# Kernel tuning notes

Hardware: AMD Instinct MI355X
Metric: run time of the kernel (lower is better)

Reference implementation:

```python
import jax, jax.numpy as jnp
import numpy as np

D = 768  # BERT hidden / GCN feature dim


def gcn_conv(x, src, dst, W, b, num_nodes):
    """PyG GCNConv: add self-loops, symmetric normalization, x @ W, scatter-sum, + bias."""
    loop = jnp.arange(num_nodes, dtype=src.dtype)
    s = jnp.concatenate([src, loop])
    d = jnp.concatenate([dst, loop])
    deg = jax.ops.segment_sum(jnp.ones_like(d, dtype=x.dtype), d, num_segments=num_nodes)
    dis = jax.lax.rsqrt(deg)  # deg >= 1 due to self-loops
    norm = dis[s] * dis[d]  # [E+N]
    h = x @ W  # [N, out]
    msg = h[s] * norm[:, None]  # [E+N, out] -- largest intermediate
    return jax.ops.segment_sum(msg, d, num_segments=num_nodes) + b


def setup_inputs() -> dict:
    key = jax.random.key(0)
    ks = jax.random.split(key, 12)
    B, N, E, K = 64, 50000, 500000, 20
    inp = {
        "query_bert_embedding": jax.random.normal(ks[0], (B, D), jnp.float32),
        "names_bert_embedding": jax.random.normal(ks[1], (N, D), jnp.float32),
        "sparse_score": jax.random.uniform(ks[2], (B, N), jnp.float32),
        "query_indices": jax.random.randint(ks[3], (B,), 0, N, jnp.int32),
        "edge_index": jax.random.randint(ks[4], (2, E), 0, N, jnp.int32),
        "sparse_weight": jnp.ones((1,), jnp.float32),
        "W1": jax.random.normal(ks[5], (D, D), jnp.float32) * (1.0 / np.sqrt(D)),
        "b1": jnp.zeros((D,), jnp.float32),
        "W2": jax.random.normal(ks[6], (D, D), jnp.float32) * (1.0 / np.sqrt(D)),
        "b2": jnp.zeros((D,), jnp.float32),
        "score_W": jax.random.normal(ks[7], (2 * D, 1), jnp.float32) * (1.0 / np.sqrt(2 * D)),
        "score_b": jnp.zeros((1,), jnp.float32),
        "top_k": K,
    }
    return inp


def reference(query_bert_embedding, names_bert_embedding, sparse_score, query_indices,
              edge_index, sparse_weight, W1, b1, W2, b2, score_W, score_b, top_k):
    N = names_bert_embedding.shape[0]
    src, dst = edge_index[0], edge_index[1]

    # two-layer GraphSAGE (GCNConv) over the name graph (dropout omitted for determinism)
    g = gcn_conv(names_bert_embedding, src, dst, W1, b1, N)
    g = jax.nn.relu(g)
    names_graph_embedding = gcn_conv(g, src, dst, W2, b2, N)  # [N, D]

    # candidate retrieval (torch.no_grad in original)
    bert_score = query_bert_embedding @ names_bert_embedding.T  # [B, N]
    score_full = jax.lax.stop_gradient(sparse_weight[0] * sparse_score + bert_score)
    _, candidates_indices = jax.lax.top_k(score_full, top_k)  # [B, K]

    # training: force gold index into candidate list (replace last slot if absent)
    qi = query_indices.astype(candidates_indices.dtype)
    contains = jnp.any(candidates_indices == qi[:, None], axis=1)  # [B]
    candidates_indices = candidates_indices.at[:, -1].set(
        jnp.where(contains, candidates_indices[:, -1], qi))

    # vectorized per-candidate gather + concat + Linear(1536->1) + ReLU
    cand_g = names_graph_embedding[candidates_indices]  # [B, K, D]
    B, K = candidates_indices.shape
    q = jnp.broadcast_to(query_bert_embedding[:, None, :], (B, K, D))
    feat = jnp.concatenate([cand_g, q], axis=-1)  # [B, K, 2D]
    score = jax.nn.relu(jnp.squeeze(feat @ score_W, -1) + score_b[0])  # [B, K]
    return score, candidates_indices
```

## Files before the change

kernel.cpp:

```cpp
#include <hip/hip_runtime.h>
#include <stdint.h>

#define D 768
#define FCH 16
#define CPC 16
#define NCAND 256

typedef __bf16 bf16x8 __attribute__((ext_vector_type(8)));
typedef float  f32x4  __attribute__((ext_vector_type(4)));
typedef float  f32x2  __attribute__((ext_vector_type(2)));

static __device__ __forceinline__ float b2f(unsigned short u){
    union { unsigned int i; float f; } v; v.i = ((unsigned int)u) << 16; return v.f;
}
static __device__ __forceinline__ unsigned short f2b(float f){
    union { float f; unsigned int i; } v; v.f = f;
    unsigned int u = v.i;
    unsigned int r = (u + 0x7fffu + ((u >> 16) & 1u)) >> 16;
    return (unsigned short)r;
}
static __device__ __forceinline__ void gload_lds16(const void* g, void* l){
    __builtin_amdgcn_global_load_lds((const __attribute__((address_space(1))) void*)g,
                                     (__attribute__((address_space(3))) void*)l, 16, 0, 0);
}
static __device__ __forceinline__ void dec4_fma(unsigned int u, float nm, float* acc){
    f32x2 a = __builtin_amdgcn_cvt_pk_f32_fp8((int)u, false);
    f32x2 b = __builtin_amdgcn_cvt_pk_f32_fp8((int)u, true);
    acc[0] += a[0] * nm; acc[1] += a[1] * nm;
    acc[2] += b[0] * nm; acc[3] += b[1] * nm;
}
static __device__ __forceinline__ unsigned char f2fp8(float f){
    int p = __builtin_amdgcn_cvt_pk_fp8_f32(f, 0.0f, 0, false);
    return (unsigned char)(p & 0xFF);
}
static __device__ __forceinline__ unsigned int pk4_fp8(float a, float b, float c, float d){
    int lo = __builtin_amdgcn_cvt_pk_fp8_f32(a, b, 0, false);
    int fu = __builtin_amdgcn_cvt_pk_fp8_f32(c, d, lo, true);
    return (unsigned int)fu;
}

__global__ __launch_bounds__(256) void cvt8_kernel(const float* __restrict__ x,
                                                   unsigned char* __restrict__ y8, size_t n){
    size_t i = ((size_t)blockIdx.x * 256 + threadIdx.x) * 4;
    if (i + 3 < n){
        f32x4 v = *(const f32x4*)(x + i);
        *(unsigned int*)(y8 + i) = pk4_fp8(v[0], v[1], v[2], v[3]);
    }
}

__global__ __launch_bounds__(256) void transposeW8(const float* __restrict__ W,
                                                   unsigned char* __restrict__ Wt){
    __shared__ unsigned char tile[32][33];
    int bx = blockIdx.x * 32;
    int by = blockIdx.y * 32;
    int tx = threadIdx.x & 31, ty = threadIdx.x >> 5;
    #pragma unroll
    for (int r = 0; r < 32; r += 8)
        tile[ty + r][tx] = f2fp8(W[(size_t)(bx + ty + r) * D + by + tx]);
    __syncthreads();
    #pragma unroll
    for (int r = 0; r < 32; r += 8)
        Wt[(size_t)(by + ty + r) * D + bx + tx] = tile[tx][ty + r];
}

__global__ __launch_bounds__(256) void deg_count(const int* __restrict__ dst, int* cnt, int E){
    int e = blockIdx.x * 256 + threadIdx.x;
    if (e < E) atomicAdd(&cnt[dst[e]], 1);
}
__global__ __launch_bounds__(256) void dis_blocksum(const int* __restrict__ cnt,
                                                    float* __restrict__ dis,
                                                    int* __restrict__ bsum, int N){
    __shared__ int sm[256];
    int tid = threadIdx.x;
    int i = blockIdx.x * 256 + tid;
    int c = (i < N) ? cnt[i] : 0;
    if (i < N) dis[i] = rsqrtf((float)(c + 1));
    sm[tid] = c;
    __syncthreads();
    for (int o = 128; o > 0; o >>= 1){
        if (tid < o) sm[tid] += sm[tid + o];
        __syncthreads();
    }
    if (tid == 0) bsum[blockIdx.x] = sm[0];
}
__global__ __launch_bounds__(256) void scanb_k(const int* __restrict__ bsum, int* boff, int nb){
    __shared__ int sm[256];
    int tid = threadIdx.x;
    int v = (tid < nb) ? bsum[tid] : 0;
    sm[tid] = v;
    __syncthreads();
    for (int o = 1; o < 256; o <<= 1){
        int add = (tid >= o) ? sm[tid - o] : 0;
        __syncthreads();
        sm[tid] += add;
        __syncthreads();
    }
    if (tid < nb) boff[tid] = sm[tid] - v;
}
__global__ __launch_bounds__(256) void scanfin_k(const int* __restrict__ cnt,
                                                 const int* __restrict__ boff,
                                                 int* start, int* fill, int N, int E){
    __shared__ int sm[256];
    int tid = threadIdx.x;
    int i = blockIdx.x * 256 + tid;
    int v = (i < N) ? cnt[i] : 0;
    sm[tid] = v;
    __syncthreads();
    for (int o = 1; o < 256; o <<= 1){
        int add = (tid >= o) ? sm[tid - o] : 0;
        __syncthreads();
        sm[tid] += add;
        __syncthreads();
    }
    if (i < N){ start[i] = boff[blockIdx.x] + sm[tid] - v; fill[i] = 0; }
    if (i == 0) start[N] = E;
}
__global__ __launch_bounds__(256) void csr_fill(const int* __restrict__ src,
                                                const int* __restrict__ dst,
                                                const float* __restrict__ dis,
                                                const int* __restrict__ start,
                                                int* fill, int* csr_src, float* csr_norm, int E){
    int e = blockIdx.x * 256 + threadIdx.x;
    if (e >= E) return;
    int s = src[e], d = dst[e];
    int pos = atomicAdd(&fill[d], 1);
    int idx = start[d] + pos;
    csr_src[idx]  = s;
    csr_norm[idx] = dis[s] * dis[d];
}

__global__ __launch_bounds__(256) void gemm_fp8(const unsigned char* __restrict__ A,
                                                const unsigned char* __restrict__ Bt,
                                                unsigned char* __restrict__ Cout,
                                                int M, int nTilesN){
    __shared__ unsigned char Al[128 * 32];
    __shared__ unsigned char Bl[128 * 32];
    const int nwg = gridDim.x;
    const int bid = blockIdx.x;
    const int q = nwg >> 3, r = nwg & 7;
    const int xcd = bid & 7, loc = bid >> 3;
    const int swz = (xcd < r ? xcd * (q + 1) : r * (q + 1) + (xcd - r) * q) + loc;
    const int mt = swz / nTilesN, nt = swz % nTilesN;
    const int m0 = mt * 128, n0 = nt * 128;

    const int tid  = threadIdx.x;
    const int lane = tid & 63;
    const int w    = tid >> 6;
    const int wr = w >> 1, wc = w & 1;
    const int l15 = lane & 15;
    const int lg  = lane >> 4;

    const int g     = w * 64 + lane;
    const int srow  = g >> 1;
    const int shalf = (g & 1) * 16;

    f32x4 acc[4][4] = {};

    for (int k0 = 0; k0 < D; k0 += 32){
        gload_lds16(A  + (size_t)(m0 + srow) * D + k0 + shalf, (char*)Al + w * 1024);
        gload_lds16(Bt + (size_t)(n0 + srow) * D + k0 + shalf, (char*)Bl + w * 1024);
        __syncthreads();
        long af[4], bfv[4];
        #pragma unroll
        for (int mf = 0; mf < 4; mf++)
            af[mf] = *(const long*)(&Al[(wr * 64 + mf * 16 + l15) * 32 + lg * 8]);
        #pragma unroll
        for (int nf = 0; nf < 4; nf++)
            bfv[nf] = *(const long*)(&Bl[(wc * 64 + nf * 16 + l15) * 32 + lg * 8]);
        #pragma unroll
        for (int mf = 0; mf < 4; mf++)
            #pragma unroll
            for (int nf = 0; nf < 4; nf++)
                acc[mf][nf] = __builtin_amdgcn_mfma_f32_16x16x32_fp8_fp8(af[mf], bfv[nf], acc[mf][nf], 0, 0, 0);
        __syncthreads();
    }
    #pragma unroll
    for (int mf = 0; mf < 4; mf++){
        #pragma unroll
        for (int r2 = 0; r2 < 4; r2++){
            int gr = m0 + wr * 64 + mf * 16 + lg * 4 + r2;
            if (gr < M){
                #pragma unroll
                for (int nf = 0; nf < 4; nf++){
                    int gc = n0 + wc * 64 + nf * 16 + l15;
                    Cout[(size_t)gr * D + gc] = f2fp8(acc[mf][nf][r2]);
                }
            }
        }
    }
}

__global__ __launch_bounds__(256) void gemm_fp8_list(const unsigned char* __restrict__ A,
                                                     const unsigned char* __restrict__ Bt,
                                                     unsigned char* __restrict__ Cout,
                                                     const int* __restrict__ RL,
                                                     const int* __restrict__ rcp,
                                                     int nTilesN){
    const int rc = *rcp;
    __shared__ unsigned char Al[128 * 32];
    __shared__ unsigned char Bl[128 * 32];
    __shared__ int rlTile[128];
    const int nwg = gridDim.x;
    const int bid = blockIdx.x;
    const int q = nwg >> 3, r = nwg & 7;
    const int xcd = bid & 7, loc = bid >> 3;
    const int swz = (xcd < r ? xcd * (q + 1) : r * (q + 1) + (xcd - r) * q) + loc;
    const int mt = swz / nTilesN, nt = swz % nTilesN;
    const int m0 = mt * 128, n0 = nt * 128;
    if (m0 >= rc) return;

    const int tid  = threadIdx.x;
    if (tid < 128){
        int p = m0 + tid;
        rlTile[tid] = RL[p < rc ? p : rc - 1];
    }
    const int lane = tid & 63;
    const int w    = tid >> 6;
    const int wr = w >> 1, wc = w & 1;
    const int l15 = lane & 15;
    const int lg  = lane >> 4;

    const int g     = w * 64 + lane;
    const int srow  = g >> 1;
    const int shalf = (g & 1) * 16;
    __syncthreads();
    const int arow = rlTile[srow];

    f32x4 acc[4][4] = {};

    for (int k0 = 0; k0 < D; k0 += 32){
        gload_lds16(A  + (size_t)arow * D + k0 + shalf, (char*)Al + w * 1024);
        gload_lds16(Bt + (size_t)(n0 + srow) * D + k0 + shalf, (char*)Bl + w * 1024);
        __syncthreads();
        long af[4], bfv[4];
        #pragma unroll
        for (int mf = 0; mf < 4; mf++)
            af[mf] = *(const long*)(&Al[(wr * 64 + mf * 16 + l15) * 32 + lg * 8]);
        #pragma unroll
        for (int nf = 0; nf < 4; nf++)
            bfv[nf] = *(const long*)(&Bl[(wc * 64 + nf * 16 + l15) * 32 + lg * 8]);
        #pragma unroll
        for (int mf = 0; mf < 4; mf++)
            #pragma unroll
            for (int nf = 0; nf < 4; nf++)
                acc[mf][nf] = __builtin_amdgcn_mfma_f32_16x16x32_fp8_fp8(af[mf], bfv[nf], acc[mf][nf], 0, 0, 0);
        __syncthreads();
    }
    #pragma unroll
    for (int mf = 0; mf < 4; mf++){
        #pragma unroll
        for (int r2 = 0; r2 < 4; r2++){
            int lr = wr * 64 + mf * 16 + lg * 4 + r2;
            if (m0 + lr < rc){
                int gr = rlTile[lr];
                #pragma unroll
                for (int nf = 0; nf < 4; nf++){
                    int gc = n0 + wc * 64 + nf * 16 + l15;
                    Cout[(size_t)gr * D + gc] = f2fp8(acc[mf][nf][r2]);
                }
            }
        }
    }
}

template<bool OUT8, bool LIST>
__global__ __launch_bounds__(256) void agg_fp8(const unsigned char* __restrict__ h8,
                                               void* __restrict__ out,
                                               const int* __restrict__ start,
                                               const int* __restrict__ csr_src,
                                               const float* __restrict__ csr_norm,
                                               const float* __restrict__ dis,
                                               const float* __restrict__ bias,
                                               const int* __restrict__ list,
                                               const int* __restrict__ Mp,
                                               int doRelu, int M){
    if (Mp) M = *Mp;
    int pair = blockIdx.x * 4 + (threadIdx.x >> 6);
    if (pair >= M) return;
    int wid = LIST ? list[pair] : pair;
    int lane = threadIdx.x & 63;
    const int lo = lane * 12;
    float acc[12] = {};
    float dn = dis[wid];
    float sn = dn * dn;
    {
        const unsigned char* hr = h8 + (size_t)wid * D + lo;
        unsigned int u0 = *(const unsigned int*)(hr);
        unsigned int u1 = *(const unsigned int*)(hr + 4);
        unsigned int u2 = *(const unsigned int*)(hr + 8);
        dec4_fma(u0, sn, acc); dec4_fma(u1, sn, acc + 4); dec4_fma(u2, sn, acc + 8);
    }
    int e0 = start[wid], e1 = start[wid + 1];
    int e = e0;
    for (; e + 8 <= e1; e += 8){
        int s[8]; float nm[8]; unsigned int u[8][3];
        #pragma unroll
        for (int b = 0; b < 8; b++){ s[b] = csr_src[e + b]; nm[b] = csr_norm[e + b]; }
        #pragma unroll
        for (int b = 0; b < 8; b++){
            const unsigned char* hs = h8 + (size_t)s[b] * D + lo;
            u[b][0] = *(const unsigned int*)(hs);
            u[b][1] = *(const unsigned int*)(hs + 4);
            u[b][2] = *(const unsigned int*)(hs + 8);
        }
        #pragma unroll
        for (int b = 0; b < 8; b++){
            dec4_fma(u[b][0], nm[b], acc);
            dec4_fma(u[b][1], nm[b], acc + 4);
            dec4_fma(u[b][2], nm[b], acc + 8);
        }
    }
    for (; e < e1; e++){
        int s = csr_src[e];
        float nm = csr_norm[e];
        const unsigned char* hs = h8 + (size_t)s * D + lo;
        unsigned int u0 = *(const unsigned int*)(hs);
        unsigned int u1 = *(const unsigned int*)(hs + 4);
        unsigned int u2 = *(const unsigned int*)(hs + 8);
        dec4_fma(u0, nm, acc); dec4_fma(u1, nm, acc + 4); dec4_fma(u2, nm, acc + 8);
    }
    float r[12];
    #pragma unroll
    for (int i = 0; i < 12; i++){
        float t = acc[i] + bias[lo + i];
        if (doRelu) t = fmaxf(t, 0.0f);
        r[i] = t;
    }
    if constexpr (OUT8){
        unsigned char* orow = (unsigned char*)out + (size_t)wid * D + lo;
        #pragma unroll
        for (int j = 0; j < 3; j++)
            *(unsigned int*)(orow + j * 4) = pk4_fp8(r[j*4], r[j*4+1], r[j*4+2], r[j*4+3]);
    } else {
        unsigned short* orow = (unsigned short*)out + (size_t)wid * D + lo;
        #pragma unroll
        for (int j = 0; j < 3; j++){
            unsigned long long packed =
                (unsigned long long)f2b(r[j*4+0]) |
                ((unsigned long long)f2b(r[j*4+1]) << 16) |
                ((unsigned long long)f2b(r[j*4+2]) << 32) |
                ((unsigned long long)f2b(r[j*4+3]) << 48);
            __builtin_nontemporal_store(packed, (unsigned long long*)(orow + j * 4));
        }
    }
}

__global__ __launch_bounds__(256) void mark_rows(const int* __restrict__ cand,
                                                 const int* __restrict__ start,
                                                 const int* __restrict__ csr_src,
                                                 int* __restrict__ flag, int M){
    int i = blockIdx.x * 4 + (threadIdx.x >> 6);
    if (i >= M) return;
    int lane = threadIdx.x & 63;
    int c = cand[i];
    if (lane == 0) flag[c] = 1;
    int e0 = start[c], e1 = start[c + 1];
    for (int e = e0 + lane; e < e1; e += 64) flag[csr_src[e]] = 1;
}
__global__ __launch_bounds__(256) void compact_rows(const int* __restrict__ flag,
                                                    int* __restrict__ RL, int* rc, int N){
    int i = blockIdx.x * 256 + threadIdx.x;
    if (i < N && flag[i]) RL[atomicAdd(rc, 1)] = i;
}

__global__ __launch_bounds__(256) void mfma_bert8(const unsigned char* __restrict__ Q8,
                                                  const unsigned char* __restrict__ X8,
                                                  const float* __restrict__ sparse,
                                                  const float* __restrict__ swp,
                                                  float* __restrict__ scoreOut,
                                                  int B, int N){
    __shared__ unsigned char Al[64 * 32];
    __shared__ unsigned char Bl[128 * 32];
    const int tid  = threadIdx.x;
    const int lane = tid & 63;
    const int w    = tid >> 6;
    const int l15  = lane & 15;
    const int lg   = lane >> 4;
    const int n0   = blockIdx.x * 128;

    const int ga    = tid;
    const int arow  = ga >> 1;
    const int ahalf = (ga & 1) * 16;
    const int gb    = w * 64 + lane;
    const int brow  = gb >> 1;
    const int bhalf = (gb & 1) * 16;

    f32x4 acc[4][2] = {};

    for (int k0 = 0; k0 < D; k0 += 32){
        if (w < 2)
            gload_lds16(Q8 + (size_t)arow * D + k0 + ahalf, (char*)Al + w * 1024);
        gload_lds16(X8 + (size_t)(n0 + brow) * D + k0 + bhalf, (char*)Bl + w * 1024);
        __syncthreads();
        long af[4], bfv[2];
        #pragma unroll
        for (int mf = 0; mf < 4; mf++)
            af[mf] = *(const long*)(&Al[(mf * 16 + l15) * 32 + lg * 8]);
        #pragma unroll
        for (int nf = 0; nf < 2; nf++)
            bfv[nf] = *(const long*)(&Bl[(w * 32 + nf * 16 + l15) * 32 + lg * 8]);
        #pragma unroll
        for (int mf = 0; mf < 4; mf++)
            #pragma unroll
            for (int nf = 0; nf < 2; nf++)
                acc[mf][nf] = __builtin_amdgcn_mfma_f32_16x16x32_fp8_fp8(af[mf], bfv[nf], acc[mf][nf], 0, 0, 0);
        __syncthreads();
    }
    float sw = swp[0];
    #pragma unroll
    for (int mf = 0; mf < 4; mf++){
        #pragma unroll
        for (int nf = 0; nf < 2; nf++){
            #pragma unroll
            for (int r = 0; r < 4; r++){
                int q = mf * 16 + lg * 4 + r;
                int n = n0 + w * 32 + nf * 16 + l15;
                if (q < B && n < N)
                    scoreOut[(size_t)q * N + n] = sw * sparse[(size_t)q * N + n] + acc[mf][nf][r];
            }
        }
    }
}

__global__ __launch_bounds__(256) void filter_topc(const float* __restrict__ score,
                                                   int* __restrict__ candIdx,
                                                   int N, int chunk){
    int b = blockIdx.y, g = blockIdx.x, tid = threadIdx.x;
    int base = g * chunk;
    const float* s = score + (size_t)b * N;
    extern __shared__ float vals[];
    for (int i = tid; i < chunk; i += 256){
        int n = base + i;
        vals[i] = (n < N) ? s[n] : -3.0e38f;
    }
    __shared__ float wv[4];
    __shared__ int   wsl[4];
    __syncthreads();
    int lane = tid & 63, wid = tid >> 6;
    int* out = candIdx + ((size_t)b * gridDim.x + g) * CPC;
    for (int it = 0; it < CPC; it++){
        float best = -3.0e38f; int bs = 0x7fffffff;
        for (int i = tid; i < chunk; i += 256){
            float v = vals[i];
            if (v > best){ best = v; bs = i; }
        }
        #pragma unroll
        for (int o = 32; o > 0; o >>= 1){
            float v2 = __shfl_down(best, o);
            int   s2 = __shfl_down(bs, o);
            if (v2 > best || (v2 == best && s2 < bs)){ best = v2; bs = s2; }
        }
        if (lane == 0){ wv[wid] = best; wsl[wid] = bs; }
        __syncthreads();
        if (tid == 0){
            float bv = wv[0]; int bi = wsl[0];
            #pragma unroll
            for (int w2 = 1; w2 < 4; w2++)
                if (wv[w2] > bv || (wv[w2] == bv && wsl[w2] < bi)){ bv = wv[w2]; bi = wsl[w2]; }
            out[it] = base + bi;
            if (bi >= 0 && bi < chunk) vals[bi] = -3.0e38f;
        }
        __syncthreads();
    }
}

__global__ __launch_bounds__(256) void rescore_kernel(const float* __restrict__ Q,
                                                      const float* __restrict__ X,
                                                      const float* __restrict__ sparse,
                                                      const float* __restrict__ swp,
                                                      const int* __restrict__ candIdx,
                                                      float* __restrict__ resVal,
                                                      int N){
    int b = blockIdx.y;
    int c0 = blockIdx.x * 64;
    int lane = threadIdx.x & 63, w = threadIdx.x >> 6;
    const float* q = Q + (size_t)b * D;
    f32x4 qv[3];
    #pragma unroll
    for (int j = 0; j < 3; j++) qv[j] = *(const f32x4*)(q + lane * 4 + 256 * j);
    float sw = swp[0];
    for (int t = 0; t < 16; t++){
        int ci = c0 + w * 16 + t;
        int n = candIdx[(size_t)b * NCAND + ci];
        const float* x = X + (size_t)n * D;
        float sum = 0.0f;
        #pragma unroll
        for (int j = 0; j < 3; j++){
            f32x4 xv = *(const f32x4*)(x + lane * 4 + 256 * j);
            sum += qv[j][0]*xv[0] + qv[j][1]*xv[1] + qv[j][2]*xv[2] + qv[j][3]*xv[3];
        }
        #pragma unroll
        for (int o = 32; o > 0; o >>= 1) sum += __shfl_down(sum, o);
        if (lane == 0)
            resVal[(size_t)b * NCAND + ci] = sw * sparse[(size_t)b * N + n] + sum;
    }
}

__global__ __launch_bounds__(256) void select_topk(const float* __restrict__ resVal,
                                                   const int* __restrict__ candIdx,
                                                   const int* __restrict__ qidx,
                                                   int* __restrict__ cand,
                                                   float* __restrict__ outIdx,
                                                   int K){
    int b = blockIdx.x, tid = threadIdx.x;
    __shared__ float vals[NCAND];
    __shared__ int   gidx[NCAND];
    __shared__ int   csel[64];
    __shared__ float wv[4];
    __shared__ int   wi[4];
    __shared__ int   wsl[4];
    vals[tid] = resVal[(size_t)b * NCAND + tid];
    gidx[tid] = candIdx[(size_t)b * NCAND + tid];
    __syncthreads();
    int lane = tid & 63, wid = tid >> 6;
    for (int it = 0; it < K; it++){
        float best = vals[tid]; int bg = gidx[tid]; int bsl = tid;
        #pragma unroll
        for (int o = 32; o > 0; o >>= 1){
            float v2 = __shfl_down(best, o);
            int   g2 = __shfl_down(bg, o);
            int   s2 = __shfl_down(bsl, o);
            if (v2 > best || (v2 == best && g2 < bg)){ best = v2; bg = g2; bsl = s2; }
        }
        if (lane == 0){ wv[wid] = best; wi[wid] = bg; wsl[wid] = bsl; }
        __syncthreads();
        if (tid == 0){
            float bv = wv[0]; int bi = wi[0]; int sl = wsl[0];
            #pragma unroll
            for (int w2 = 1; w2 < 4; w2++)
                if (wv[w2] > bv || (wv[w2] == bv && wi[w2] < bi)){ bv = wv[w2]; bi = wi[w2]; sl = wsl[w2]; }
            csel[it] = bi;
            vals[sl] = -3.0e38f;
        }
        __syncthreads();
    }
    if (tid == 0){
        int qi = qidx[b];
        bool has = false;
        for (int k2 = 0; k2 < K; k2++) if (csel[k2] == qi) has = true;
        if (!has) csel[K - 1] = qi;
    }
    __syncthreads();
    if (tid < K){
        cand[b * K + tid]   = csel[tid];
        outIdx[b * K + tid] = (float)csel[tid];
    }
}

__global__ __launch_bounds__(256) void final_kernel(const unsigned short* __restrict__ emb,
                                                    const float* __restrict__ Q,
                                                    const int* __restrict__ cand,
                                                    const float* __restrict__ scoreW,
                                                    const float* __restrict__ scoreB,
                                                    float* __restrict__ out, int B, int K){
    int pair = blockIdx.x * 4 + (threadIdx.x >> 6);
    if (pair >= B * K) return;
    int lane = threadIdx.x & 63;
    int b = pair / K;
    int c = cand[pair];
    const unsigned short* g = emb + (size_t)c * D;
    const float* q = Q + (size_t)b * D;
    float sum = 0.0f;
    #pragma unroll
    for (int j = 0; j < 12; j++){
        int col = lane + 64 * j;
        sum += b2f(g[col]) * scoreW[col] + q[col] * scoreW[D + col];
    }
    #pragma unroll
    for (int o = 32; o > 0; o >>= 1) sum += __shfl_down(sum, o);
    if (lane == 0) out[pair] = fmaxf(sum + scoreB[0], 0.0f);
}

extern "C" void kernel_launch(void* const* d_in, const int* in_sizes, int n_in,
                              void* d_out, int out_size, void* d_ws, size_t ws_size,
                              hipStream_t stream){
    const float* q_emb   = (const float*)d_in[0];
    const float* x_emb   = (const float*)d_in[1];
    const float* sparse  = (const float*)d_in[2];
    const int*   q_idx   = (const int*)d_in[3];
    const int*   eidx    = (const int*)d_in[4];
    const float* sweight = (const float*)d_in[5];
    const float* W1      = (const float*)d_in[6];
    const float* b1      = (const float*)d_in[7];
    const float* W2      = (const float*)d_in[8];
    const float* b2      = (const float*)d_in[9];
    const float* scoreW  = (const float*)d_in[10];
    const float* scoreB  = (const float*)d_in[11];

    const int B = in_sizes[0] / D;
    const int N = in_sizes[1] / D;
    const int E = in_sizes[4] / 2;
    const int K = out_size / (2 * B);

    const int* esrc = eidx;
    const int* edst = eidx + E;

    char* ws = (char*)d_ws;
    size_t off = 0;
    auto alloc = [&](size_t bytes) -> char* {
        char* p = ws + off;
        off = (off + bytes + 255) & ~(size_t)255;
        return p;
    };
    unsigned char*  bufX8 = (unsigned char*)alloc((size_t)(N + 128) * D);
    unsigned char*  bufH8 = (unsigned char*)alloc((size_t)(N + 128) * D);
    unsigned char*  bufG8 = (unsigned char*)alloc((size_t)(N + 128) * D);
    unsigned short* bufG  = (unsigned short*)alloc((size_t)N * D * 2);
    unsigned char*  Qb8   = (unsigned char*)alloc((size_t)(B + 64) * D);
    unsigned char*  W1t8  = (unsigned char*)alloc((size_t)D * D);
    unsigned char*  W2t8  = (unsigned char*)alloc((size_t)D * D);
    int*   cnt   = (int*)alloc((size_t)N * 4);
    float* dis   = (float*)alloc((size_t)N * 4);
    int*   start = (int*)alloc((size_t)(N + 1) * 4);
    int*   fill  = (int*)alloc((size_t)N * 4);
    int*   bsum  = (int*)alloc(1024);
    int*   boff  = (int*)alloc(1024);
    int*   csrs  = (int*)alloc((size_t)E * 4);
    float* csrn  = (float*)alloc((size_t)E * 4);
    float* approxScore = (float*)alloc((size_t)B * N * 4);
    int*   candIdx = (int*)alloc((size_t)B * NCAND * 4);
    float* resVal  = (float*)alloc((size_t)B * NCAND * 4);
    int*   candBuf = (int*)alloc((size_t)B * K * 4);
    int*   flag    = (int*)alloc((size_t)N * 4);
    int*   RL      = (int*)alloc((size_t)(N + 128) * 4);
    int*   rcp     = (int*)alloc(256);
    (void)ws_size; (void)n_in;

    float* outScore = (float*)d_out;
    float* outIdx   = outScore + (size_t)B * K;

    size_t nx = (size_t)N * D;
    cvt8_kernel<<<(unsigned)((nx / 4 + 255) / 256), 256, 0, stream>>>(x_emb, bufX8, nx);
    size_t nq = (size_t)B * D;
    cvt8_kernel<<<(unsigned)((nq / 4 + 255) / 256), 256, 0, stream>>>(q_emb, Qb8, nq);
    dim3 tg(D / 32, D / 32);
    transposeW8<<<tg, 256, 0, stream>>>(W1, W1t8);
    transposeW8<<<tg, 256, 0, stream>>>(W2, W2t8);

    int nb = (N + 255) / 256;
    hipMemsetAsync(cnt, 0, (size_t)N * 4, stream);
    deg_count<<<(E + 255) / 256, 256, 0, stream>>>(edst, cnt, E);
    dis_blocksum<<<nb, 256, 0, stream>>>(cnt, dis, bsum, N);
    scanb_k<<<1, 256, 0, stream>>>(bsum, boff, nb);
    scanfin_k<<<nb, 256, 0, stream>>>(cnt, boff, start, fill, N, E);
    csr_fill<<<(E + 255) / 256, 256, 0, stream>>>(esrc, edst, dis, start, fill, csrs, csrn, E);

    mfma_bert8<<<(N + 127) / 128, 256, 0, stream>>>(Qb8, bufX8, sparse, sweight, approxScore, B, N);
    int chunk = (N + FCH - 1) / FCH;
    dim3 fgrid(FCH, B);
    filter_topc<<<fgrid, 256, (size_t)chunk * 4, stream>>>(approxScore, candIdx, N, chunk);
    dim3 rgrid(NCAND / 64, B);
    rescore_kernel<<<rgrid, 256, 0, stream>>>(q_emb, x_emb, sparse, sweight, candIdx, resVal, N);
    select_topk<<<B, 256, 0, stream>>>(resVal, candIdx, q_idx, candBuf, outIdx, K);

    hipMemsetAsync(flag, 0, (size_t)N * 4, stream);
    hipMemsetAsync(rcp, 0, 4, stream);
    mark_rows<<<(B * K + 3) / 4, 256, 0, stream>>>(candBuf, start, csrs, flag, B * K);
    compact_rows<<<nb, 256, 0, stream>>>(flag, RL, rcp, N);

    const int nTilesM = (N + 127) / 128;
    const int nTilesN = D / 128;
    const int gemmWG  = nTilesM * nTilesN;
    gemm_fp8<<<gemmWG, 256, 0, stream>>>(bufX8, W1t8, bufH8, N, nTilesN);
    agg_fp8<true, true><<<(N + 3) / 4, 256, 0, stream>>>(bufH8, bufG8, start, csrs, csrn, dis, b1, RL, rcp, 1, N);

    gemm_fp8_list<<<gemmWG, 256, 0, stream>>>(bufG8, W2t8, bufH8, RL, rcp, nTilesN);
    agg_fp8<false, true><<<(B * K + 3) / 4, 256, 0, stream>>>(bufH8, bufG, start, csrs, csrn, dis, b2, candBuf, nullptr, 0, B * K);

    final_kernel<<<(B * K + 3) / 4, 256, 0, stream>>>(bufG, q_emb, candBuf, scoreW, scoreB, outScore, B, K);
}
```

Baseline: 406.8 us.

## Merge prep launches and double the K-step in fp8 GEMMs

Merges the two fp8 conversion launches into one kernel and the two weight transposes into one launch with a z-dimension. Replaces three memsets with a single zeroing kernel. Both fp8 GEMMs now stage a 64-wide K slice per iteration instead of 32, which halves the barrier count per tile and uses more shared memory. The aim is less launch overhead and less synchronisation per GEMM, at the cost of larger LDS tiles that may lower occupancy.

```diff
diff --git a/kernel.cpp b/kernel.cpp
--- a/kernel.cpp
+++ b/kernel.cpp
@@ -39,17 +39,27 @@
     return (unsigned int)fu;
 }
 
-__global__ __launch_bounds__(256) void cvt8_kernel(const float* __restrict__ x,
-                                                   unsigned char* __restrict__ y8, size_t n){
-    size_t i = ((size_t)blockIdx.x * 256 + threadIdx.x) * 4;
-    if (i + 3 < n){
-        f32x4 v = *(const f32x4*)(x + i);
-        *(unsigned int*)(y8 + i) = pk4_fp8(v[0], v[1], v[2], v[3]);
-    }
-}
-
-__global__ __launch_bounds__(256) void transposeW8(const float* __restrict__ W,
-                                                   unsigned char* __restrict__ Wt){
+__global__ __launch_bounds__(256) void cvt8_fused(const float* __restrict__ x,
+                                                  unsigned char* __restrict__ y8, size_t nxq,
+                                                  const float* __restrict__ qq,
+                                                  unsigned char* __restrict__ q8, size_t nqq){
+    size_t i = (size_t)blockIdx.x * 256 + threadIdx.x;
+    if (i < nxq){
+        f32x4 v = *(const f32x4*)(x + i * 4);
+        *(unsigned int*)(y8 + i * 4) = pk4_fp8(v[0], v[1], v[2], v[3]);
+    } else if (i - nxq < nqq){
+        size_t j = i - nxq;
+        f32x4 v = *(const f32x4*)(qq + j * 4);
+        *(unsigned int*)(q8 + j * 4) = pk4_fp8(v[0], v[1], v[2], v[3]);
+    }
+}
+
+__global__ __launch_bounds__(256) void transposeW8(const float* __restrict__ W1,
+                                                   unsigned char* __restrict__ W1t,
+                                                   const float* __restrict__ W2,
+                                                   unsigned char* __restrict__ W2t){
+    const float* W = blockIdx.z ? W2 : W1;
+    unsigned char* Wt = blockIdx.z ? W2t : W1t;
     __shared__ unsigned char tile[32][33];
     int bx = blockIdx.x * 32;
     int by = blockIdx.y * 32;
@@ -61,6 +71,13 @@
     #pragma unroll
     for (int r = 0; r < 32; r += 8)
         Wt[(size_t)(by + ty + r) * D + bx + tx] = tile[tx][ty + r];
+}
+
+__global__ __launch_bounds__(256) void prep_zero(int* __restrict__ cnt, int* __restrict__ flag,
+                                                 int* __restrict__ rcp, int N){
+    int i = blockIdx.x * 256 + threadIdx.x;
+    if (i < N){ cnt[i] = 0; flag[i] = 0; }
+    if (i == 0) rcp[0] = 0;
 }
 
 __global__ __launch_bounds__(256) void deg_count(const int* __restrict__ dst, int* cnt, int E){
@@ -133,8 +150,8 @@
                                                 const unsigned char* __restrict__ Bt,
                                                 unsigned char* __restrict__ Cout,
                                                 int M, int nTilesN){
-    __shared__ unsigned char Al[128 * 32];
-    __shared__ unsigned char Bl[128 * 32];
+    __shared__ unsigned char Al[128 * 64];
+    __shared__ unsigned char Bl[128 * 64];
     const int nwg = gridDim.x;
     const int bid = blockIdx.x;
     const int q = nwg >> 3, r = nwg & 7;
@@ -150,28 +167,32 @@
     const int l15 = lane & 15;
     const int lg  = lane >> 4;
 
-    const int g     = w * 64 + lane;
-    const int srow  = g >> 1;
-    const int shalf = (g & 1) * 16;
+    const int row0 = tid >> 2,        q0 = (tid & 3) * 16;
+    const int row1 = (tid + 256) >> 2, q1 = ((tid + 256) & 3) * 16;
 
     f32x4 acc[4][4] = {};
 
-    for (int k0 = 0; k0 < D; k0 += 32){
-        gload_lds16(A  + (size_t)(m0 + srow) * D + k0 + shalf, (char*)Al + w * 1024);
-        gload_lds16(Bt + (size_t)(n0 + srow) * D + k0 + shalf, (char*)Bl + w * 1024);
-        __syncthreads();
-        long af[4], bfv[4];
-        #pragma unroll
-        for (int mf = 0; mf < 4; mf++)
-            af[mf] = *(const long*)(&Al[(wr * 64 + mf * 16 + l15) * 32 + lg * 8]);
-        #pragma unroll
-        for (int nf = 0; nf < 4; nf++)
-            bfv[nf] = *(const long*)(&Bl[(wc * 64 + nf * 16 + l15) * 32 + lg * 8]);
-        #pragma unroll
-        for (int mf = 0; mf < 4; mf++)
+    for (int k0 = 0; k0 < D; k0 += 64){
+        gload_lds16(A  + (size_t)(m0 + row0) * D + k0 + q0, (char*)Al + tid * 16);
+        gload_lds16(A  + (size_t)(m0 + row1) * D + k0 + q1, (char*)Al + (tid + 256) * 16);
+        gload_lds16(Bt + (size_t)(n0 + row0) * D + k0 + q0, (char*)Bl + tid * 16);
+        gload_lds16(Bt + (size_t)(n0 + row1) * D + k0 + q1, (char*)Bl + (tid + 256) * 16);
+        __syncthreads();
+        #pragma unroll
+        for (int ks = 0; ks < 2; ks++){
+            long af[4], bfv[4];
+            #pragma unroll
+            for (int mf = 0; mf < 4; mf++)
+                af[mf] = *(const long*)(&Al[(wr * 64 + mf * 16 + l15) * 64 + ks * 32 + lg * 8]);
             #pragma unroll
             for (int nf = 0; nf < 4; nf++)
-                acc[mf][nf] = __builtin_amdgcn_mfma_f32_16x16x32_fp8_fp8(af[mf], bfv[nf], acc[mf][nf], 0, 0, 0);
+                bfv[nf] = *(const long*)(&Bl[(wc * 64 + nf * 16 + l15) * 64 + ks * 32 + lg * 8]);
+            #pragma unroll
+            for (int mf = 0; mf < 4; mf++)
+                #pragma unroll
+                for (int nf = 0; nf < 4; nf++)
+                    acc[mf][nf] = __builtin_amdgcn_mfma_f32_16x16x32_fp8_fp8(af[mf], bfv[nf], acc[mf][nf], 0, 0, 0);
+        }
         __syncthreads();
     }
     #pragma unroll
@@ -197,8 +218,8 @@
                                                      const int* __restrict__ rcp,
                                                      int nTilesN){
     const int rc = *rcp;
-    __shared__ unsigned char Al[128 * 32];
-    __shared__ unsigned char Bl[128 * 32];
+    __shared__ unsigned char Al[128 * 64];
+    __shared__ unsigned char Bl[128 * 64];
     __shared__ int rlTile[128];
     const int nwg = gridDim.x;
     const int bid = blockIdx.x;
@@ -220,30 +241,35 @@
     const int l15 = lane & 15;
     const int lg  = lane >> 4;
 
-    const int g     = w * 64 + lane;
-    const int srow  = g >> 1;
-    const int shalf = (g & 1) * 16;
-    __syncthreads();
-    const int arow = rlTile[srow];
+    const int row0 = tid >> 2,        q0 = (tid & 3) * 16;
+    const int row1 = (tid + 256) >> 2, q1 = ((tid + 256) & 3) * 16;
+    __syncthreads();
+    const int arow0 = rlTile[row0];
+    const int arow1 = rlTile[row1];
 
     f32x4 acc[4][4] = {};
 
-    for (int k0 = 0; k0 < D; k0 += 32){
-        gload_lds16(A  + (size_t)arow * D + k0 + shalf, (char*)Al + w * 1024);
-        gload_lds16(Bt + (size_t)(n0 + srow) * D + k0 + shalf, (char*)Bl + w * 1024);
-        __syncthreads();
-        long af[4], bfv[4];
-        #pragma unroll
-        for (int mf = 0; mf < 4; mf++)
-            af[mf] = *(const long*)(&Al[(wr * 64 + mf * 16 + l15) * 32 + lg * 8]);
-        #pragma unroll
-        for (int nf = 0; nf < 4; nf++)
-            bfv[nf] = *(const long*)(&Bl[(wc * 64 + nf * 16 + l15) * 32 + lg * 8]);
-        #pragma unroll
-        for (int mf = 0; mf < 4; mf++)
+    for (int k0 = 0; k0 < D; k0 += 64){
+        gload_lds16(A  + (size_t)arow0 * D + k0 + q0, (char*)Al + tid * 16);
+        gload_lds16(A  + (size_t)arow1 * D + k0 + q1, (char*)Al + (tid + 256) * 16);
+        gload_lds16(Bt + (size_t)(n0 + row0) * D + k0 + q0, (char*)Bl + tid * 16);
+        gload_lds16(Bt + (size_t)(n0 + row1) * D + k0 + q1, (char*)Bl + (tid + 256) * 16);
+        __syncthreads();
+        #pragma unroll
+        for (int ks = 0; ks < 2; ks++){
+            long af[4], bfv[4];
+            #pragma unroll
+            for (int mf = 0; mf < 4; mf++)
+                af[mf] = *(const long*)(&Al[(wr * 64 + mf * 16 + l15) * 64 + ks * 32 + lg * 8]);
             #pragma unroll
             for (int nf = 0; nf < 4; nf++)
-                acc[mf][nf] = __builtin_amdgcn_mfma_f32_16x16x32_fp8_fp8(af[mf], bfv[nf], acc[mf][nf], 0, 0, 0);
+                bfv[nf] = *(const long*)(&Bl[(wc * 64 + nf * 16 + l15) * 64 + ks * 32 + lg * 8]);
+            #pragma unroll
+            for (int mf = 0; mf < 4; mf++)
+                #pragma unroll
+                for (int nf = 0; nf < 4; nf++)
+                    acc[mf][nf] = __builtin_amdgcn_mfma_f32_16x16x32_fp8_fp8(af[mf], bfv[nf], acc[mf][nf], 0, 0, 0);
+        }
         __syncthreads();
     }
     #pragma unroll
@@ -629,16 +655,14 @@
     float* outScore = (float*)d_out;
     float* outIdx   = outScore + (size_t)B * K;
 
-    size_t nx = (size_t)N * D;
-    cvt8_kernel<<<(unsigned)((nx / 4 + 255) / 256), 256, 0, stream>>>(x_emb, bufX8, nx);
-    size_t nq = (size_t)B * D;
-    cvt8_kernel<<<(unsigned)((nq / 4 + 255) / 256), 256, 0, stream>>>(q_emb, Qb8, nq);
-    dim3 tg(D / 32, D / 32);
-    transposeW8<<<tg, 256, 0, stream>>>(W1, W1t8);
-    transposeW8<<<tg, 256, 0, stream>>>(W2, W2t8);
+    size_t nxq = (size_t)N * D / 4;
+    size_t nqq = (size_t)B * D / 4;
+    cvt8_fused<<<(unsigned)((nxq + nqq + 255) / 256), 256, 0, stream>>>(x_emb, bufX8, nxq, q_emb, Qb8, nqq);
+    dim3 tg(D / 32, D / 32, 2);
+    transposeW8<<<tg, 256, 0, stream>>>(W1, W1t8, W2, W2t8);
 
     int nb = (N + 255) / 256;
-    hipMemsetAsync(cnt, 0, (size_t)N * 4, stream);
+    prep_zero<<<nb, 256, 0, stream>>>(cnt, flag, rcp, N);
     deg_count<<<(E + 255) / 256, 256, 0, stream>>>(edst, cnt, E);
     dis_blocksum<<<nb, 256, 0, stream>>>(cnt, dis, bsum, N);
     scanb_k<<<1, 256, 0, stream>>>(bsum, boff, nb);
@@ -653,8 +677,6 @@
     rescore_kernel<<<rgrid, 256, 0, stream>>>(q_emb, x_emb, sparse, sweight, candIdx, resVal, N);
     select_topk<<<B, 256, 0, stream>>>(resVal, candIdx, q_idx, candBuf, outIdx, K);
 
-    hipMemsetAsync(flag, 0, (size_t)N * 4, stream);
-    hipMemsetAsync(rcp, 0, 4, stream);
     mark_rows<<<(B * K + 3) / 4, 256, 0, stream>>>(candBuf, start, csrs, flag, B * K);
     compact_rows<<<nb, 256, 0, stream>>>(flag, RL, rcp, N);
 
```

After: 446.4 us. +9.7%, slower.
